# Optimization experiments

Hardware: AMD Instinct MI355X
Metric: run time of the kernel (lower is better)

The kernel has to match this reference:

```python
import jax, jax.numpy as jnp
import numpy as np

K = 512  # num codes
COMMITMENT_COST = 0.25

def setup_inputs() -> dict:
    key = jax.random.key(0)
    k1, k2 = jax.random.split(key)
    z = jax.random.normal(k1, (64, 64, 64, 64), dtype=jnp.float32)   # (B, C=D, H, W)
    emb = jax.random.normal(k2, (K, 64), dtype=jnp.float32)          # codebook (K, D)
    return {"z": z, "emb": emb}

def reference(z, emb):
    B, C, H, W = z.shape
    z_nhwc = jnp.transpose(z, (0, 2, 3, 1))            # (B, H, W, C)
    zf = z_nhwc.reshape(-1, C)                          # (BHW, C)
    # squared-distance matrix: ||z||^2 + ||e||^2 - 2 z.e  -> (BHW, K)
    dist = (jnp.sum(zf * zf, axis=1, keepdims=True)
            + jnp.sum(emb * emb, axis=1)
            - 2.0 * jnp.einsum('bd,kd->bk', zf, emb))
    idx = jnp.argmin(dist, axis=1)                      # (BHW,)
    enc = jax.nn.one_hot(idx, K, dtype=z.dtype)         # (BHW, K)
    avg_use = jnp.mean(enc, axis=0)
    perplexity = jnp.exp(-jnp.sum(avg_use * jnp.log(avg_use + 1e-10)))
    z_q = emb[idx].reshape(B, H, W, C)                  # gathered codes
    sg = jax.lax.stop_gradient
    loss = (COMMITMENT_COST * jnp.mean((sg(z_q) - z_nhwc) ** 2)
            + jnp.mean((z_q - sg(z_nhwc)) ** 2))
    z_q_ste = z_nhwc + sg(z_q - z_nhwc)                 # straight-through
    z_q_out = jnp.transpose(z_q_ste, (0, 3, 1, 2))      # (B, C, H, W)
    idx_out = idx.reshape(B, H, W)
    return z_q_out, loss, idx_out, perplexity
```

## Files before the change

kernel.cpp:

```cpp
#include <hip/hip_runtime.h>

#define ZQ_OFF    0
#define LOSS_OFF  16777216
#define IDX_OFF   16777217
#define PERP_OFF  17039361

#define NPOINTS   262144
#define NELEM     16777216


typedef float sf16 __attribute__((ext_vector_type(16)));
typedef float sf4  __attribute__((ext_vector_type(4)));

#define SLOAD5(E0,E1,E2,E3,EN,GB,NB,O0,O1,O2,O3)       \
  asm("s_load_dwordx16 %0, %5, " O0 "\n\t"             \
      "s_load_dwordx16 %1, %5, " O1 "\n\t"             \
      "s_load_dwordx16 %2, %5, " O2 "\n\t"             \
      "s_load_dwordx16 %3, %5, " O3 "\n\t"             \
      "s_load_dwordx4  %4, %6, 0x0\n\t"                \
      "s_waitcnt lgkmcnt(0)"                           \
      : "=s"(E0), "=s"(E1), "=s"(E2), "=s"(E3), "=s"(EN) \
      : "s"(GB), "s"(NB))

#define SLOAD4(E0,E1,E2,E3,GB,O0,O1,O2,O3)             \
  asm("s_load_dwordx16 %0, %4, " O0 "\n\t"             \
      "s_load_dwordx16 %1, %4, " O1 "\n\t"             \
      "s_load_dwordx16 %2, %4, " O2 "\n\t"             \
      "s_load_dwordx16 %3, %4, " O3 "\n\t"             \
      "s_waitcnt lgkmcnt(0)"                           \
      : "=s"(E0), "=s"(E1), "=s"(E2), "=s"(E3)         \
      : "s"(GB))

#define FMACHUNK(E0,E1,E2,E3,DC)                        \
  { _Pragma("unroll")                                   \
    for (int j = 0; j < 16; ++j) {                      \
      float v = zv[(DC) + j];                           \
      a0 += v * E0[j];                                  \
      a1 += v * E1[j];                                  \
      a2 += v * E2[j];                                  \
      a3 += v * E3[j];                                  \
    } }

__global__ void prep_kernel(const float* __restrict__ emb,
                            float* __restrict__ embnorm,
                            int* __restrict__ hist,
                            double* __restrict__ lossacc) {
    int k = threadIdx.x;
    hist[k] = 0;
    const float* e = emb + (k << 6);
    float s = 0.f;
    #pragma unroll
    for (int d = 0; d < 64; ++d) s += e[d] * e[d];
    embnorm[k] = s;
    if (k == 0) *lossacc = 0.0;
}

__global__ __launch_bounds__(256)
__attribute__((amdgpu_waves_per_eu(4, 4)))
void vq_kernel(const float* __restrict__ z,
               const float* __restrict__ emb,
               const float* __restrict__ embnorm,
               float* __restrict__ out,
               int* __restrict__ hist,
               double* __restrict__ lossacc) {
    const int bid = blockIdx.x;
    const int b  = bid >> 4;
    const int h  = ((bid & 15) << 2) + (threadIdx.x >> 6);
    const int w  = threadIdx.x & 63;

    const float* zp = z + ((size_t)b << 18) + ((size_t)h << 6) + w;
    float zv[64];
    float z2 = 0.f;
    #pragma unroll
    for (int d = 0; d < 64; ++d) {
        float v = zp[(size_t)d << 12];
        zv[d] = v;
        z2 += v * v;
    }
    #pragma unroll
    for (int d = 0; d < 64; ++d) {
        asm volatile("" : "+v"(zv[d]));
    }

    float best = 3.4e38f;
    int   bidx = 0;
    #pragma unroll 1
    for (int k0 = 0; k0 < 512; k0 += 4) {
        const float* gb = emb + ((size_t)k0 << 6);
        const float* nb = embnorm + k0;
        sf16 E0, E1, E2, E3;
        sf4  EN;
        float a0 = 0.f, a1 = 0.f, a2 = 0.f, a3 = 0.f;

        SLOAD5(E0, E1, E2, E3, EN, gb, nb, "0x0",  "0x100", "0x200", "0x300");
        FMACHUNK(E0, E1, E2, E3, 0)
        SLOAD4(E0, E1, E2, E3, gb,        "0x40", "0x140", "0x240", "0x340");
        FMACHUNK(E0, E1, E2, E3, 16)
        SLOAD4(E0, E1, E2, E3, gb,        "0x80", "0x180", "0x280", "0x380");
        FMACHUNK(E0, E1, E2, E3, 32)
        SLOAD4(E0, E1, E2, E3, gb,        "0xC0", "0x1C0", "0x2C0", "0x3C0");
        FMACHUNK(E0, E1, E2, E3, 48)

        float d0 = z2 + EN[0] - 2.f * a0;
        float d1 = z2 + EN[1] - 2.f * a1;
        float d2 = z2 + EN[2] - 2.f * a2;
        float d3 = z2 + EN[3] - 2.f * a3;
        if (d0 < best) { best = d0; bidx = k0;     }
        if (d1 < best) { best = d1; bidx = k0 + 1; }
        if (d2 < best) { best = d2; bidx = k0 + 2; }
        if (d3 < best) { best = d3; bidx = k0 + 3; }
    }

    const size_t pidx = ((size_t)b << 12) + ((size_t)h << 6) + w;
    __builtin_nontemporal_store((float)bidx, &out[IDX_OFF + pidx]);
    atomicAdd(&hist[bidx], 1);

    const float* eb = emb + ((size_t)bidx << 6);
    float* zqout = out + ((size_t)b << 18) + ((size_t)h << 6) + w;
    float lsum = 0.f;
    #pragma unroll
    for (int d = 0; d < 64; ++d) {
        float e    = eb[d];
        float diff = e - zv[d];
        lsum += diff * diff;
        __builtin_nontemporal_store(zv[d] + diff, &zqout[(size_t)d << 12]);
    }

    #pragma unroll
    for (int off = 32; off; off >>= 1) lsum += __shfl_down(lsum, off, 64);
    __shared__ float wsum[4];
    if ((threadIdx.x & 63) == 0) wsum[threadIdx.x >> 6] = lsum;
    __syncthreads();
    if (threadIdx.x == 0) {
        atomicAdd(lossacc, (double)(wsum[0] + wsum[1] + wsum[2] + wsum[3]));
    }
}

__global__ void fin_kernel(const int* __restrict__ hist,
                           const double* __restrict__ lossacc,
                           float* __restrict__ out) {
    int k = threadIdx.x;
    float avg = (float)hist[k] * (1.0f / 262144.0f);
    float t = avg * logf(avg + 1e-10f);
    #pragma unroll
    for (int off = 32; off; off >>= 1) t += __shfl_down(t, off, 64);
    __shared__ float s[8];
    if ((k & 63) == 0) s[k >> 6] = t;
    __syncthreads();
    if (k == 0) {
        float S = 0.f;
        #pragma unroll
        for (int i = 0; i < 8; ++i) S += s[i];
        out[PERP_OFF] = expf(-S);
        out[LOSS_OFF] = (float)(1.25 * (*lossacc) / (double)NELEM);
    }
}

extern "C" void kernel_launch(void* const* d_in, const int* in_sizes, int n_in,
                              void* d_out, int out_size, void* d_ws, size_t ws_size,
                              hipStream_t stream) {
    const float* z   = (const float*)d_in[0];
    const float* emb = (const float*)d_in[1];
    float* out = (float*)d_out;

    float*  embnorm = (float*)d_ws;
    int*    hist    = (int*)((char*)d_ws + 2048);
    double* lossacc = (double*)((char*)d_ws + 4096);

    prep_kernel<<<1, 512, 0, stream>>>(emb, embnorm, hist, lossacc);
    vq_kernel<<<1024, 256, 0, stream>>>(z, emb, embnorm, out, hist, lossacc);
    fin_kernel<<<1, 512, 0, stream>>>(hist, lossacc, out);
}
```

Measured before the change: 476.4 us.

## Split codebook search across two waves per point with LDS argmin merge

Each pixel row is now handled by two waves, each scanning half of the codebook, and the partial minima are merged through shared memory before the winning wave writes outputs. The grid doubles and the fixed waves-per-EU attribute is removed. This is meant to raise wave-level parallelism and hide scalar load latency in the distance loop. The cost is duplicated z loads, an extra barrier, and half the waves idling during the epilogue.

```diff
diff --git a/kernel.cpp b/kernel.cpp
--- a/kernel.cpp
+++ b/kernel.cpp
@@ -56,17 +56,26 @@
 }
 
 __global__ __launch_bounds__(256)
-__attribute__((amdgpu_waves_per_eu(4, 4)))
 void vq_kernel(const float* __restrict__ z,
                const float* __restrict__ emb,
                const float* __restrict__ embnorm,
                float* __restrict__ out,
                int* __restrict__ hist,
                double* __restrict__ lossacc) {
-    const int bid = blockIdx.x;
-    const int b  = bid >> 4;
-    const int h  = ((bid & 15) << 2) + (threadIdx.x >> 6);
-    const int w  = threadIdx.x & 63;
+    const int tid  = threadIdx.x;
+    const int lane = tid & 63;
+    const int wv   = __builtin_amdgcn_readfirstlane(tid >> 6);
+    const int row  = wv & 1;
+    const int half = wv >> 1;
+    const int bid  = blockIdx.x;
+    const int b    = bid >> 5;
+    const int h    = ((bid & 31) << 1) | row;
+    const int w    = lane;
+
+    __shared__ float sd[128];
+    __shared__ int   sk[128];
+    __shared__ float wsum[2];
+    const int slot = (row << 6) | lane;
 
     const float* zp = z + ((size_t)b << 18) + ((size_t)h << 6) + w;
     float zv[64];
@@ -82,10 +91,11 @@
         asm volatile("" : "+v"(zv[d]));
     }
 
+    const int kbase = half << 8;
     float best = 3.4e38f;
-    int   bidx = 0;
+    int   bidx = kbase;
     #pragma unroll 1
-    for (int k0 = 0; k0 < 512; k0 += 4) {
+    for (int k0 = kbase; k0 < kbase + 256; k0 += 4) {
         const float* gb = emb + ((size_t)k0 << 6);
         const float* nb = embnorm + k0;
         sf16 E0, E1, E2, E3;
@@ -111,28 +121,36 @@
         if (d3 < best) { best = d3; bidx = k0 + 3; }
     }
 
-    const size_t pidx = ((size_t)b << 12) + ((size_t)h << 6) + w;
-    __builtin_nontemporal_store((float)bidx, &out[IDX_OFF + pidx]);
-    atomicAdd(&hist[bidx], 1);
+    if (half == 1) { sd[slot] = best; sk[slot] = bidx; }
+    __syncthreads();
 
-    const float* eb = emb + ((size_t)bidx << 6);
-    float* zqout = out + ((size_t)b << 18) + ((size_t)h << 6) + w;
     float lsum = 0.f;
-    #pragma unroll
-    for (int d = 0; d < 64; ++d) {
-        float e    = eb[d];
-        float diff = e - zv[d];
-        lsum += diff * diff;
-        __builtin_nontemporal_store(zv[d] + diff, &zqout[(size_t)d << 12]);
+    if (half == 0) {
+        float db = sd[slot];
+        int   kb = sk[slot];
+        if (db < best) { best = db; bidx = kb; }
+
+        const size_t pidx = ((size_t)b << 12) + ((size_t)h << 6) + w;
+        __builtin_nontemporal_store((float)bidx, &out[IDX_OFF + pidx]);
+        atomicAdd(&hist[bidx], 1);
+
+        const float* eb = emb + ((size_t)bidx << 6);
+        float* zqout = out + ((size_t)b << 18) + ((size_t)h << 6) + w;
+        #pragma unroll
+        for (int d = 0; d < 64; ++d) {
+            float e    = eb[d];
+            float diff = e - zv[d];
+            lsum += diff * diff;
+            __builtin_nontemporal_store(zv[d] + diff, &zqout[(size_t)d << 12]);
+        }
+
+        #pragma unroll
+        for (int off = 32; off; off >>= 1) lsum += __shfl_down(lsum, off, 64);
+        if (lane == 0) wsum[row] = lsum;
     }
-
-    #pragma unroll
-    for (int off = 32; off; off >>= 1) lsum += __shfl_down(lsum, off, 64);
-    __shared__ float wsum[4];
-    if ((threadIdx.x & 63) == 0) wsum[threadIdx.x >> 6] = lsum;
     __syncthreads();
-    if (threadIdx.x == 0) {
-        atomicAdd(lossacc, (double)(wsum[0] + wsum[1] + wsum[2] + wsum[3]));
+    if (tid == 0) {
+        atomicAdd(lossacc, (double)(wsum[0] + wsum[1]));
     }
 }
 
@@ -168,6 +186,6 @@
     double* lossacc = (double*)((char*)d_ws + 4096);
 
     prep_kernel<<<1, 512, 0, stream>>>(emb, embnorm, hist, lossacc);
-    vq_kernel<<<1024, 256, 0, stream>>>(z, emb, embnorm, out, hist, lossacc);
+    vq_kernel<<<2048, 256, 0, stream>>>(z, emb, embnorm, out, hist, lossacc);
     fin_kernel<<<1, 512, 0, stream>>>(hist, lossacc, out);
 }
```

Result: faster. 445.0 us (-6.6%).
